# Performance work log

Hardware: AMD Instinct MI355X
Metric: run time of the kernel (lower is better)

The kernel has to match this reference:

```python
import jax, jax.numpy as jnp
import numpy as np

HALF_WIN = 6  # window_size // 2 on each side (window_size=13)


def setup_inputs() -> dict:
    key = jax.random.key(0)
    k1, k2, k3 = jax.random.split(key, 3)
    B, N, C = 2, 4096, 768
    x = jax.random.normal(k1, (B, N, C), dtype=jnp.float32)
    # torch Linear init ~ U(-1/sqrt(in), 1/sqrt(in)); stored here as [in, out]
    s = 1.0 / np.sqrt(C)
    w_qkv = jax.random.uniform(k2, (C, 3 * C), jnp.float32, -s, s)
    w_proj = jax.random.uniform(k3, (C, C), jnp.float32, -s, s)
    b_proj = jnp.zeros((C,), jnp.float32)
    return {"x": x, "w_qkv": w_qkv, "w_proj": w_proj, "b_proj": b_proj}


def _local_attn(x, w_qkv, w_proj, b_proj, num_heads=12):
    B, N, C = x.shape
    H = num_heads
    D = C // H
    W = 2 * HALF_WIN + 1  # 13

    qkv = (x @ w_qkv).reshape(B, N, 3, H, D)
    q, k, v = qkv[:, :, 0], qkv[:, :, 1], qkv[:, :, 2]  # each [B,N,H,D]

    # sliding-window gather: for each query i, keys at i-6..i+6
    offs = jnp.arange(-HALF_WIN, HALF_WIN + 1)            # [W]
    idx = jnp.arange(N)[:, None] + offs[None, :]          # [N,W]
    valid = (idx >= 0) & (idx < N)                        # [N,W]
    idxc = jnp.clip(idx, 0, N - 1)

    k_win = k[:, idxc]  # [B,N,W,H,D]
    v_win = v[:, idxc]  # [B,N,W,H,D]

    scale = D ** (-0.5)  # xformers default softmax scale
    scores = jnp.einsum('bnhd,bnwhd->bnhw', q, k_win) * scale  # [B,N,H,W]
    neg = jnp.asarray(jnp.finfo(scores.dtype).min, scores.dtype)
    scores = jnp.where(valid[None, :, None, :], scores, neg)
    p = jax.nn.softmax(scores, axis=-1)

    out = jnp.einsum('bnhw,bnwhd->bnhd', p, v_win)  # [B,N,H,D]
    out = out.reshape(B, N, C)
    return out @ w_proj + b_proj


def reference(x, w_qkv, w_proj, b_proj):
    return _local_attn(x, w_qkv, w_proj, b_proj)
```

## Files before the change

### kernel.cpp

```cpp
#include <hip/hip_runtime.h>

typedef unsigned short u16;
typedef unsigned int u32;
typedef __attribute__((ext_vector_type(8))) short short8;
typedef __attribute__((ext_vector_type(4))) float f32x4;

#define GLOBAL_AS(p) (const __attribute__((address_space(1))) void*)(p)
#define LDS_AS(p) (__attribute__((address_space(3))) void*)(p)

__device__ __forceinline__ u16 f2b(float f) {
  u32 u = __float_as_uint(f);
  u32 r = (u + 0x7fffu + ((u >> 16) & 1u)) >> 16;
  return (u16)r;
}
__device__ __forceinline__ float blo(u32 u) { return __uint_as_float(u << 16); }
__device__ __forceinline__ float bhi(u32 u) { return __uint_as_float(u & 0xffff0000u); }

__global__ void conv_bf16(const float* __restrict__ in, u16* __restrict__ out, int n4) {
  int i = blockIdx.x * blockDim.x + threadIdx.x;
  int stride = gridDim.x * blockDim.x;
  for (; i < n4; i += stride) {
    float4 f = ((const float4*)in)[i];
    ushort4 u;
    u.x = f2b(f.x); u.y = f2b(f.y); u.z = f2b(f.z); u.w = f2b(f.w);
    ((ushort4*)out)[i] = u;
  }
}

__global__ void transpose_conv2(const float* __restrict__ w_qkv, u16* __restrict__ wqT,
                                const float* __restrict__ w_proj, u16* __restrict__ wpT) {
  __shared__ float tile[32][33];
  const int z = blockIdx.z;
  if (z && blockIdx.x >= 24) return;
  const float* in = z ? w_proj : w_qkv;
  u16* out = z ? wpT : wqT;
  const int Cc = z ? 768 : 2304;
  int c0 = blockIdx.x * 32, r0 = blockIdx.y * 32;
  int tx = threadIdx.x, ty = threadIdx.y;
#pragma unroll
  for (int i = 0; i < 32; i += 8)
    tile[ty + i][tx] = in[(size_t)(r0 + ty + i) * Cc + c0 + tx];
  __syncthreads();
#pragma unroll
  for (int i = 0; i < 32; i += 8)
    out[(size_t)(c0 + ty + i) * 768 + r0 + tx] = f2b(tile[tx][ty + i]);
}


#define STAGE(KT, SB)                                                                    \
  do {                                                                                   \
    __builtin_amdgcn_global_load_lds(GLOBAL_AS(gAs + (KT) * 32),                         \
                                     LDS_AS(lA + (SB) * 4096 + t * 8), 16, 0, 0);        \
    __builtin_amdgcn_global_load_lds(GLOBAL_AS(gB0s + (KT) * 32),                        \
                                     LDS_AS(lB + (SB) * 8192 + t * 8), 16, 0, 0);        \
    __builtin_amdgcn_global_load_lds(GLOBAL_AS(gB1s + (KT) * 32),                        \
                                     LDS_AS(lB + (SB) * 8192 + (t + 512) * 8), 16, 0, 0);\
  } while (0)

#define ITER(KT, CB, SB, DOSTAGE, VM)                                                    \
  do {                                                                                   \
    asm volatile("s_waitcnt vmcnt(" VM ")" ::: "memory");                                \
    __builtin_amdgcn_s_barrier();                                                        \
    asm volatile("" ::: "memory");                                                       \
    if (DOSTAGE) STAGE((KT) + 2, SB);                                                    \
    const u16* pa_ = lA + (CB) * 4096;                                                   \
    const u16* pb_ = lB + (CB) * 8192;                                                   \
    short8 af0 = *(const short8*)(pa_ + aoff0);                                          \
    short8 af1 = *(const short8*)(pa_ + aoff1);                                          \
    short8 af2 = *(const short8*)(pa_ + aoff2);                                          \
    short8 af3 = *(const short8*)(pa_ + aoff3);                                          \
    short8 bf0 = *(const short8*)(pb_ + boff0);                                          \
    short8 bf1 = *(const short8*)(pb_ + boff1);                                          \
    short8 bf2 = *(const short8*)(pb_ + boff2);                                          \
    short8 bf3 = *(const short8*)(pb_ + boff3);                                          \
    __builtin_amdgcn_s_setprio(1);                                                       \
    acc[0][0] = __builtin_amdgcn_mfma_f32_16x16x32_bf16(af0, bf0, acc[0][0], 0, 0, 0);   \
    acc[0][1] = __builtin_amdgcn_mfma_f32_16x16x32_bf16(af0, bf1, acc[0][1], 0, 0, 0);   \
    acc[0][2] = __builtin_amdgcn_mfma_f32_16x16x32_bf16(af0, bf2, acc[0][2], 0, 0, 0);   \
    acc[0][3] = __builtin_amdgcn_mfma_f32_16x16x32_bf16(af0, bf3, acc[0][3], 0, 0, 0);   \
    acc[1][0] = __builtin_amdgcn_mfma_f32_16x16x32_bf16(af1, bf0, acc[1][0], 0, 0, 0);   \
    acc[1][1] = __builtin_amdgcn_mfma_f32_16x16x32_bf16(af1, bf1, acc[1][1], 0, 0, 0);   \
    acc[1][2] = __builtin_amdgcn_mfma_f32_16x16x32_bf16(af1, bf2, acc[1][2], 0, 0, 0);   \
    acc[1][3] = __builtin_amdgcn_mfma_f32_16x16x32_bf16(af1, bf3, acc[1][3], 0, 0, 0);   \
    acc[2][0] = __builtin_amdgcn_mfma_f32_16x16x32_bf16(af2, bf0, acc[2][0], 0, 0, 0);   \
    acc[2][1] = __builtin_amdgcn_mfma_f32_16x16x32_bf16(af2, bf1, acc[2][1], 0, 0, 0);   \
    acc[2][2] = __builtin_amdgcn_mfma_f32_16x16x32_bf16(af2, bf2, acc[2][2], 0, 0, 0);   \
    acc[2][3] = __builtin_amdgcn_mfma_f32_16x16x32_bf16(af2, bf3, acc[2][3], 0, 0, 0);   \
    acc[3][0] = __builtin_amdgcn_mfma_f32_16x16x32_bf16(af3, bf0, acc[3][0], 0, 0, 0);   \
    acc[3][1] = __builtin_amdgcn_mfma_f32_16x16x32_bf16(af3, bf1, acc[3][1], 0, 0, 0);   \
    acc[3][2] = __builtin_amdgcn_mfma_f32_16x16x32_bf16(af3, bf2, acc[3][2], 0, 0, 0);   \
    acc[3][3] = __builtin_amdgcn_mfma_f32_16x16x32_bf16(af3, bf3, acc[3][3], 0, 0, 0);   \
    __builtin_amdgcn_s_setprio(0);                                                       \
    asm volatile("" ::: "memory");                                                       \
  } while (0)

template <int EPI>
__global__ __launch_bounds__(512, 4) void gemm3r(
    const u16* __restrict__ A, const u16* __restrict__ Bt, void* __restrict__ Cout,
    const float* __restrict__ bias, int M, int N, int K, int NX) {
  extern __shared__ u16 sm[];
  u16* lA = sm;
  u16* lB = sm + 3 * 4096;
  const int t = threadIdx.x;
  const int nwg = gridDim.x;
  const int logical = (blockIdx.x & 7) * (nwg >> 3) + (blockIdx.x >> 3);
  const int m0 = (logical / NX) * 128;
  const int n0 = (logical % NX) * 256;
  const int wv = t >> 6, l = t & 63;
  const int wm = wv >> 2, wn = wv & 3;
  const int lr = l & 15, g = l >> 4;

  const int ra = t >> 2;
  const int ca = (t & 3) ^ ((ra >> 1) & 3);
  const u16* gAs = A + (size_t)(m0 + ra) * K + ca * 8;
  const u16* gB0s = Bt + (size_t)(n0 + ra) * K + ca * 8;
  const u16* gB1s = Bt + (size_t)(n0 + ra + 128) * K + ca * 8;

  const int cswz = (g ^ ((lr >> 1) & 3)) * 8;
  const int ar = wm * 64 + lr;
  const int br = wn * 64 + lr;
  const int aoff0 = (ar + 0) * 32 + cswz, aoff1 = (ar + 16) * 32 + cswz;
  const int aoff2 = (ar + 32) * 32 + cswz, aoff3 = (ar + 48) * 32 + cswz;
  const int boff0 = (br + 0) * 32 + cswz, boff1 = (br + 16) * 32 + cswz;
  const int boff2 = (br + 32) * 32 + cswz, boff3 = (br + 48) * 32 + cswz;

  f32x4 acc[4][4] = {};

  STAGE(0, 0);
  STAGE(1, 1);
  for (int j = 0; j < 7; ++j) {
    const int kt = j * 3;
    ITER(kt + 0, 0, 2, 1, "3");
    ITER(kt + 1, 1, 0, 1, "3");
    ITER(kt + 2, 2, 1, 1, "3");
  }
  ITER(21, 0, 2, 1, "3");
  ITER(22, 1, 2, 0, "3");
  ITER(23, 2, 2, 0, "0");

#pragma unroll
  for (int mi = 0; mi < 4; ++mi) {
    int row = m0 + wm * 64 + mi * 16 + g * 4;
#pragma unroll
    for (int ni = 0; ni < 4; ++ni) {
      int col = n0 + wn * 64 + ni * 16 + lr;
#pragma unroll
      for (int r = 0; r < 4; ++r) {
        float v = acc[mi][ni][r];
        if (EPI == 0) {
          ((u16*)Cout)[(size_t)(row + r) * N + col] = f2b(v);
        } else {
          ((float*)Cout)[(size_t)(row + r) * N + col] = v + bias[col];
        }
      }
    }
  }
}

#define NTILE 128
#define ROWS 140
#define LPAD 66

__global__ __launch_bounds__(128) void attn_kernel(const u16* __restrict__ qkv,
                                                   u16* __restrict__ attn) {
  const int nt = blockIdx.x, h = blockIdx.y, b = blockIdx.z;
  const int n0 = nt * NTILE;
  const int t = threadIdx.x;
  __shared__ u16 kl[ROWS * LPAD];
  __shared__ u16 vl[ROWS * LPAD];

  for (int i = t; i < 2 * ROWS * 8; i += 128) {
    int mat = i >= ROWS * 8;
    int j = mat ? i - ROWS * 8 : i;
    int r = j >> 3, c = j & 7;
    int grow = n0 - 6 + r;
    grow = grow < 0 ? 0 : (grow > 4095 ? 4095 : grow);
    const uint4 u =
        *(const uint4*)(qkv + (size_t)(b * 4096 + grow) * 2304 + (mat ? 1536 : 768) + h * 64 + c * 8);
    u16* dst = (mat ? vl : kl) + r * LPAD + c * 8;
    ((u32*)dst)[0] = u.x;
    ((u32*)dst)[1] = u.y;
    ((u32*)dst)[2] = u.z;
    ((u32*)dst)[3] = u.w;
  }
  __syncthreads();

  const int wv = t >> 6, l = t & 63;
  const int n = n0 + wv * 64 + l;
  const int lrow = wv * 64 + l;

  float qf[64];
  const u16* qp = qkv + (size_t)(b * 4096 + n) * 2304 + h * 64;
#pragma unroll
  for (int c = 0; c < 8; ++c) {
    uint4 u = *(const uint4*)(qp + c * 8);
    qf[c * 8 + 0] = blo(u.x); qf[c * 8 + 1] = bhi(u.x);
    qf[c * 8 + 2] = blo(u.y); qf[c * 8 + 3] = bhi(u.y);
    qf[c * 8 + 4] = blo(u.z); qf[c * 8 + 5] = bhi(u.z);
    qf[c * 8 + 6] = blo(u.w); qf[c * 8 + 7] = bhi(u.w);
  }

  float s[13];
#pragma unroll
  for (int w = 0; w < 13; ++w) s[w] = 0.f;
#pragma unroll
  for (int d2 = 0; d2 < 32; ++d2) {
    float q0 = qf[2 * d2], q1 = qf[2 * d2 + 1];
#pragma unroll
    for (int w = 0; w < 13; ++w) {
      u32 u = *(const u32*)(kl + (lrow + w) * LPAD + 2 * d2);
      s[w] += q0 * blo(u) + q1 * bhi(u);
    }
  }

#pragma unroll
  for (int w = 0; w < 13; ++w) {
    int nn = n - 6 + w;
    s[w] = (nn >= 0 && nn < 4096) ? s[w] * 0.125f : -1e30f;
  }
  float m = s[0];
#pragma unroll
  for (int w = 1; w < 13; ++w) m = fmaxf(m, s[w]);
  float sum = 0.f;
#pragma unroll
  for (int w = 0; w < 13; ++w) {
    float p = __expf(s[w] - m);
    s[w] = p;
    sum += p;
  }
  float inv = 1.0f / sum;

  float o[64];
#pragma unroll
  for (int d = 0; d < 64; ++d) o[d] = 0.f;
#pragma unroll
  for (int w = 0; w < 13; ++w) {
    float pw = s[w] * inv;
#pragma unroll
    for (int d2 = 0; d2 < 32; ++d2) {
      u32 u = *(const u32*)(vl + (lrow + w) * LPAD + 2 * d2);
      o[2 * d2] += pw * blo(u);
      o[2 * d2 + 1] += pw * bhi(u);
    }
  }

  u16* op = attn + (size_t)(b * 4096 + n) * 768 + h * 64;
#pragma unroll
  for (int c = 0; c < 8; ++c) {
    uint4 u;
    u.x = (u32)f2b(o[c * 8 + 0]) | ((u32)f2b(o[c * 8 + 1]) << 16);
    u.y = (u32)f2b(o[c * 8 + 2]) | ((u32)f2b(o[c * 8 + 3]) << 16);
    u.z = (u32)f2b(o[c * 8 + 4]) | ((u32)f2b(o[c * 8 + 5]) << 16);
    u.w = (u32)f2b(o[c * 8 + 6]) | ((u32)f2b(o[c * 8 + 7]) << 16);
    ((uint4*)op)[c] = u;
  }
}

extern "C" void kernel_launch(void* const* d_in, const int* in_sizes, int n_in,
                              void* d_out, int out_size, void* d_ws, size_t ws_size,
                              hipStream_t stream) {
  const float* x = (const float*)d_in[0];
  const float* w_qkv = (const float*)d_in[1];
  const float* w_proj = (const float*)d_in[2];
  const float* b_proj = (const float*)d_in[3];
  float* out = (float*)d_out;

  char* p = (char*)d_ws;
  u16* xb = (u16*)p;     p += (size_t)8192 * 768 * 2;
  u16* wqT = (u16*)p;    p += (size_t)2304 * 768 * 2;
  u16* wpT = (u16*)p;    p += (size_t)768 * 768 * 2;
  u16* qkvb = (u16*)p;   p += (size_t)8192 * 2304 * 2;
  u16* attnb = (u16*)p;  p += (size_t)8192 * 768 * 2;

  const int dynlds = 72 * 1024;
  hipFuncSetAttribute((const void*)gemm3r<0>, hipFuncAttributeMaxDynamicSharedMemorySize, dynlds);
  hipFuncSetAttribute((const void*)gemm3r<1>, hipFuncAttributeMaxDynamicSharedMemorySize, dynlds);

  conv_bf16<<<dim3(1024), dim3(256), 0, stream>>>(x, xb, 8192 * 768 / 4);
  transpose_conv2<<<dim3(72, 24, 2), dim3(32, 8), 0, stream>>>(w_qkv, wqT, w_proj, wpT);

  gemm3r<0><<<dim3(9 * 64), dim3(512), dynlds, stream>>>(
      xb, wqT, (void*)qkvb, nullptr, 8192, 2304, 768, 9);

  attn_kernel<<<dim3(4096 / NTILE, 12, 2), dim3(128), 0, stream>>>(qkvb, attnb);

  gemm3r<1><<<dim3(3 * 64), dim3(512), dynlds, stream>>>(
      attnb, wpT, (void*)out, b_proj, 8192, 768, 768, 3);
}
```

Measured before the change: 179.2 us.

## Double GEMM K-tile depth to 64 with 8-way swizzled LDS layout

The bf16 MFMA GEMM now stages 64-wide K slices per pipeline step instead of 32, halving the number of barrier/wait iterations from 24 to 12. Each step issues six async global-to-LDS loads, uses an 8-chunk XOR swizzle, and runs two rounds of 16 MFMAs per barrier. LDS per block rises to 144 KB, so occupancy bounds drop from 4 to 2 blocks per CU. The activation conversion kernel's grid is also doubled.

```diff
diff --git a/kernel.cpp b/kernel.cpp
--- a/kernel.cpp
+++ b/kernel.cpp
@@ -47,60 +47,79 @@
 }
 
 
-#define STAGE(KT, SB)                                                                    \
+#define STAGE64(KT, SB)                                                                   \
+  do {                                                                                    \
+    __builtin_amdgcn_global_load_lds(GLOBAL_AS(gA0 + (KT) * 64),                          \
+                                     LDS_AS(lA + (SB) * 8192 + t * 8), 16, 0, 0);         \
+    __builtin_amdgcn_global_load_lds(GLOBAL_AS(gA1 + (KT) * 64),                          \
+                                     LDS_AS(lA + (SB) * 8192 + (t + 512) * 8), 16, 0, 0); \
+    __builtin_amdgcn_global_load_lds(GLOBAL_AS(gB0 + (KT) * 64),                          \
+                                     LDS_AS(lB + (SB) * 16384 + t * 8), 16, 0, 0);        \
+    __builtin_amdgcn_global_load_lds(GLOBAL_AS(gB1 + (KT) * 64),                          \
+                                     LDS_AS(lB + (SB) * 16384 + (t + 512) * 8), 16, 0, 0);\
+    __builtin_amdgcn_global_load_lds(GLOBAL_AS(gB2 + (KT) * 64),                          \
+                                     LDS_AS(lB + (SB) * 16384 + (t + 1024) * 8), 16, 0, 0);\
+    __builtin_amdgcn_global_load_lds(GLOBAL_AS(gB3 + (KT) * 64),                          \
+                                     LDS_AS(lB + (SB) * 16384 + (t + 1536) * 8), 16, 0, 0);\
+  } while (0)
+
+#define MFMA16(AK0, AK1, AK2, AK3, BK0, BK1, BK2, BK3)                                   \
   do {                                                                                   \
-    __builtin_amdgcn_global_load_lds(GLOBAL_AS(gAs + (KT) * 32),                         \
-                                     LDS_AS(lA + (SB) * 4096 + t * 8), 16, 0, 0);        \
-    __builtin_amdgcn_global_load_lds(GLOBAL_AS(gB0s + (KT) * 32),                        \
-                                     LDS_AS(lB + (SB) * 8192 + t * 8), 16, 0, 0);        \
-    __builtin_amdgcn_global_load_lds(GLOBAL_AS(gB1s + (KT) * 32),                        \
-                                     LDS_AS(lB + (SB) * 8192 + (t + 512) * 8), 16, 0, 0);\
+    __builtin_amdgcn_s_setprio(1);                                                       \
+    acc[0][0] = __builtin_amdgcn_mfma_f32_16x16x32_bf16(AK0, BK0, acc[0][0], 0, 0, 0);   \
+    acc[0][1] = __builtin_amdgcn_mfma_f32_16x16x32_bf16(AK0, BK1, acc[0][1], 0, 0, 0);   \
+    acc[0][2] = __builtin_amdgcn_mfma_f32_16x16x32_bf16(AK0, BK2, acc[0][2], 0, 0, 0);   \
+    acc[0][3] = __builtin_amdgcn_mfma_f32_16x16x32_bf16(AK0, BK3, acc[0][3], 0, 0, 0);   \
+    acc[1][0] = __builtin_amdgcn_mfma_f32_16x16x32_bf16(AK1, BK0, acc[1][0], 0, 0, 0);   \
+    acc[1][1] = __builtin_amdgcn_mfma_f32_16x16x32_bf16(AK1, BK1, acc[1][1], 0, 0, 0);   \
+    acc[1][2] = __builtin_amdgcn_mfma_f32_16x16x32_bf16(AK1, BK2, acc[1][2], 0, 0, 0);   \
+    acc[1][3] = __builtin_amdgcn_mfma_f32_16x16x32_bf16(AK1, BK3, acc[1][3], 0, 0, 0);   \
+    acc[2][0] = __builtin_amdgcn_mfma_f32_16x16x32_bf16(AK2, BK0, acc[2][0], 0, 0, 0);   \
+    acc[2][1] = __builtin_amdgcn_mfma_f32_16x16x32_bf16(AK2, BK1, acc[2][1], 0, 0, 0);   \
+    acc[2][2] = __builtin_amdgcn_mfma_f32_16x16x32_bf16(AK2, BK2, acc[2][2], 0, 0, 0);   \
+    acc[2][3] = __builtin_amdgcn_mfma_f32_16x16x32_bf16(AK2, BK3, acc[2][3], 0, 0, 0);   \
+    acc[3][0] = __builtin_amdgcn_mfma_f32_16x16x32_bf16(AK3, BK0, acc[3][0], 0, 0, 0);   \
+    acc[3][1] = __builtin_amdgcn_mfma_f32_16x16x32_bf16(AK3, BK1, acc[3][1], 0, 0, 0);   \
+    acc[3][2] = __builtin_amdgcn_mfma_f32_16x16x32_bf16(AK3, BK2, acc[3][2], 0, 0, 0);   \
+    acc[3][3] = __builtin_amdgcn_mfma_f32_16x16x32_bf16(AK3, BK3, acc[3][3], 0, 0, 0);   \
+    __builtin_amdgcn_s_setprio(0);                                                       \
   } while (0)
 
-#define ITER(KT, CB, SB, DOSTAGE, VM)                                                    \
+#define ITER64(KT, CB, SB, DOSTAGE, VM)                                                  \
   do {                                                                                   \
     asm volatile("s_waitcnt vmcnt(" VM ")" ::: "memory");                                \
     __builtin_amdgcn_s_barrier();                                                        \
     asm volatile("" ::: "memory");                                                       \
-    if (DOSTAGE) STAGE((KT) + 2, SB);                                                    \
-    const u16* pa_ = lA + (CB) * 4096;                                                   \
-    const u16* pb_ = lB + (CB) * 8192;                                                   \
-    short8 af0 = *(const short8*)(pa_ + aoff0);                                          \
-    short8 af1 = *(const short8*)(pa_ + aoff1);                                          \
-    short8 af2 = *(const short8*)(pa_ + aoff2);                                          \
-    short8 af3 = *(const short8*)(pa_ + aoff3);                                          \
-    short8 bf0 = *(const short8*)(pb_ + boff0);                                          \
-    short8 bf1 = *(const short8*)(pb_ + boff1);                                          \
-    short8 bf2 = *(const short8*)(pb_ + boff2);                                          \
-    short8 bf3 = *(const short8*)(pb_ + boff3);                                          \
-    __builtin_amdgcn_s_setprio(1);                                                       \
-    acc[0][0] = __builtin_amdgcn_mfma_f32_16x16x32_bf16(af0, bf0, acc[0][0], 0, 0, 0);   \
-    acc[0][1] = __builtin_amdgcn_mfma_f32_16x16x32_bf16(af0, bf1, acc[0][1], 0, 0, 0);   \
-    acc[0][2] = __builtin_amdgcn_mfma_f32_16x16x32_bf16(af0, bf2, acc[0][2], 0, 0, 0);   \
-    acc[0][3] = __builtin_amdgcn_mfma_f32_16x16x32_bf16(af0, bf3, acc[0][3], 0, 0, 0);   \
-    acc[1][0] = __builtin_amdgcn_mfma_f32_16x16x32_bf16(af1, bf0, acc[1][0], 0, 0, 0);   \
-    acc[1][1] = __builtin_amdgcn_mfma_f32_16x16x32_bf16(af1, bf1, acc[1][1], 0, 0, 0);   \
-    acc[1][2] = __builtin_amdgcn_mfma_f32_16x16x32_bf16(af1, bf2, acc[1][2], 0, 0, 0);   \
-    acc[1][3] = __builtin_amdgcn_mfma_f32_16x16x32_bf16(af1, bf3, acc[1][3], 0, 0, 0);   \
-    acc[2][0] = __builtin_amdgcn_mfma_f32_16x16x32_bf16(af2, bf0, acc[2][0], 0, 0, 0);   \
-    acc[2][1] = __builtin_amdgcn_mfma_f32_16x16x32_bf16(af2, bf1, acc[2][1], 0, 0, 0);   \
-    acc[2][2] = __builtin_amdgcn_mfma_f32_16x16x32_bf16(af2, bf2, acc[2][2], 0, 0, 0);   \
-    acc[2][3] = __builtin_amdgcn_mfma_f32_16x16x32_bf16(af2, bf3, acc[2][3], 0, 0, 0);   \
-    acc[3][0] = __builtin_amdgcn_mfma_f32_16x16x32_bf16(af3, bf0, acc[3][0], 0, 0, 0);   \
-    acc[3][1] = __builtin_amdgcn_mfma_f32_16x16x32_bf16(af3, bf1, acc[3][1], 0, 0, 0);   \
-    acc[3][2] = __builtin_amdgcn_mfma_f32_16x16x32_bf16(af3, bf2, acc[3][2], 0, 0, 0);   \
-    acc[3][3] = __builtin_amdgcn_mfma_f32_16x16x32_bf16(af3, bf3, acc[3][3], 0, 0, 0);   \
-    __builtin_amdgcn_s_setprio(0);                                                       \
-    asm volatile("" ::: "memory");                                                       \
+    if (DOSTAGE) STAGE64((KT) + 2, SB);                                                  \
+    const u16* pa_ = lA + (CB) * 8192;                                                   \
+    const u16* pb_ = lB + (CB) * 16384;                                                  \
+    short8 a0 = *(const short8*)(pa_ + arow0 + cs0);                                     \
+    short8 a1 = *(const short8*)(pa_ + arow1 + cs0);                                     \
+    short8 a2 = *(const short8*)(pa_ + arow2 + cs0);                                     \
+    short8 a3 = *(const short8*)(pa_ + arow3 + cs0);                                     \
+    short8 b0 = *(const short8*)(pb_ + brow0 + cs0);                                     \
+    short8 b1 = *(const short8*)(pb_ + brow1 + cs0);                                     \
+    short8 b2 = *(const short8*)(pb_ + brow2 + cs0);                                     \
+    short8 b3 = *(const short8*)(pb_ + brow3 + cs0);                                     \
+    MFMA16(a0, a1, a2, a3, b0, b1, b2, b3);                                              \
+    short8 c0v = *(const short8*)(pa_ + arow0 + cs1);                                    \
+    short8 c1v = *(const short8*)(pa_ + arow1 + cs1);                                    \
+    short8 c2v = *(const short8*)(pa_ + arow2 + cs1);                                    \
+    short8 c3v = *(const short8*)(pa_ + arow3 + cs1);                                    \
+    short8 d0v = *(const short8*)(pb_ + brow0 + cs1);                                    \
+    short8 d1v = *(const short8*)(pb_ + brow1 + cs1);                                    \
+    short8 d2v = *(const short8*)(pb_ + brow2 + cs1);                                    \
+    short8 d3v = *(const short8*)(pb_ + brow3 + cs1);                                    \
+    MFMA16(c0v, c1v, c2v, c3v, d0v, d1v, d2v, d3v);                                      \
   } while (0)
 
 template <int EPI>
-__global__ __launch_bounds__(512, 4) void gemm3r(
+__global__ __launch_bounds__(512, 2) void gemm64(
     const u16* __restrict__ A, const u16* __restrict__ Bt, void* __restrict__ Cout,
     const float* __restrict__ bias, int M, int N, int K, int NX) {
   extern __shared__ u16 sm[];
   u16* lA = sm;
-  u16* lB = sm + 3 * 4096;
+  u16* lB = sm + 3 * 8192;
   const int t = threadIdx.x;
   const int nwg = gridDim.x;
   const int logical = (blockIdx.x & 7) * (nwg >> 3) + (blockIdx.x >> 3);
@@ -110,33 +129,35 @@
   const int wm = wv >> 2, wn = wv & 3;
   const int lr = l & 15, g = l >> 4;
 
-  const int ra = t >> 2;
-  const int ca = (t & 3) ^ ((ra >> 1) & 3);
-  const u16* gAs = A + (size_t)(m0 + ra) * K + ca * 8;
-  const u16* gB0s = Bt + (size_t)(n0 + ra) * K + ca * 8;
-  const u16* gB1s = Bt + (size_t)(n0 + ra + 128) * K + ca * 8;
-
-  const int cswz = (g ^ ((lr >> 1) & 3)) * 8;
-  const int ar = wm * 64 + lr;
-  const int br = wn * 64 + lr;
-  const int aoff0 = (ar + 0) * 32 + cswz, aoff1 = (ar + 16) * 32 + cswz;
-  const int aoff2 = (ar + 32) * 32 + cswz, aoff3 = (ar + 48) * 32 + cswz;
-  const int boff0 = (br + 0) * 32 + cswz, boff1 = (br + 16) * 32 + cswz;
-  const int boff2 = (br + 32) * 32 + cswz, boff3 = (br + 48) * 32 + cswz;
+  const int ra = t >> 3;
+  const int ca = (t & 7) ^ (ra & 7);
+  const u16* gA0 = A + (size_t)(m0 + ra) * K + ca * 8;
+  const u16* gA1 = A + (size_t)(m0 + ra + 64) * K + ca * 8;
+  const u16* gB0 = Bt + (size_t)(n0 + ra) * K + ca * 8;
+  const u16* gB1 = Bt + (size_t)(n0 + ra + 64) * K + ca * 8;
+  const u16* gB2 = Bt + (size_t)(n0 + ra + 128) * K + ca * 8;
+  const u16* gB3 = Bt + (size_t)(n0 + ra + 192) * K + ca * 8;
+
+  const int cs0 = ((g + 0) ^ (lr & 7)) * 8;
+  const int cs1 = ((g + 4) ^ (lr & 7)) * 8;
+  const int arow0 = (wm * 64 + lr + 0) * 64, arow1 = (wm * 64 + lr + 16) * 64;
+  const int arow2 = (wm * 64 + lr + 32) * 64, arow3 = (wm * 64 + lr + 48) * 64;
+  const int brow0 = (wn * 64 + lr + 0) * 64, brow1 = (wn * 64 + lr + 16) * 64;
+  const int brow2 = (wn * 64 + lr + 32) * 64, brow3 = (wn * 64 + lr + 48) * 64;
 
   f32x4 acc[4][4] = {};
 
-  STAGE(0, 0);
-  STAGE(1, 1);
-  for (int j = 0; j < 7; ++j) {
+  STAGE64(0, 0);
+  STAGE64(1, 1);
+  for (int j = 0; j < 3; ++j) {
     const int kt = j * 3;
-    ITER(kt + 0, 0, 2, 1, "3");
-    ITER(kt + 1, 1, 0, 1, "3");
-    ITER(kt + 2, 2, 1, 1, "3");
-  }
-  ITER(21, 0, 2, 1, "3");
-  ITER(22, 1, 2, 0, "3");
-  ITER(23, 2, 2, 0, "0");
+    ITER64(kt + 0, 0, 2, 1, "6");
+    ITER64(kt + 1, 1, 0, 1, "6");
+    ITER64(kt + 2, 2, 1, 1, "6");
+  }
+  ITER64(9, 0, 2, 1, "6");
+  ITER64(10, 1, 2, 0, "6");
+  ITER64(11, 2, 2, 0, "0");
 
 #pragma unroll
   for (int mi = 0; mi < 4; ++mi) {
@@ -272,18 +293,18 @@
   u16* qkvb = (u16*)p;   p += (size_t)8192 * 2304 * 2;
   u16* attnb = (u16*)p;  p += (size_t)8192 * 768 * 2;
 
-  const int dynlds = 72 * 1024;
-  hipFuncSetAttribute((const void*)gemm3r<0>, hipFuncAttributeMaxDynamicSharedMemorySize, dynlds);
-  hipFuncSetAttribute((const void*)gemm3r<1>, hipFuncAttributeMaxDynamicSharedMemorySize, dynlds);
-
-  conv_bf16<<<dim3(1024), dim3(256), 0, stream>>>(x, xb, 8192 * 768 / 4);
+  const int dynlds = 144 * 1024;
+  hipFuncSetAttribute((const void*)gemm64<0>, hipFuncAttributeMaxDynamicSharedMemorySize, dynlds);
+  hipFuncSetAttribute((const void*)gemm64<1>, hipFuncAttributeMaxDynamicSharedMemorySize, dynlds);
+
+  conv_bf16<<<dim3(2048), dim3(256), 0, stream>>>(x, xb, 8192 * 768 / 4);
   transpose_conv2<<<dim3(72, 24, 2), dim3(32, 8), 0, stream>>>(w_qkv, wqT, w_proj, wpT);
 
-  gemm3r<0><<<dim3(9 * 64), dim3(512), dynlds, stream>>>(
+  gemm64<0><<<dim3(9 * 64), dim3(512), dynlds, stream>>>(
       xb, wqT, (void*)qkvb, nullptr, 8192, 2304, 768, 9);
 
   attn_kernel<<<dim3(4096 / NTILE, 12, 2), dim3(128), 0, stream>>>(qkvb, attnb);
 
-  gemm3r<1><<<dim3(3 * 64), dim3(512), dynlds, stream>>>(
+  gemm64<1><<<dim3(3 * 64), dim3(512), dynlds, stream>>>(
       attnb, wpT, (void*)out, b_proj, 8192, 768, 768, 3);
 }
```

Result: no change. 178.7 us (-0.2%).
